# Optimization experiments

Measured on AMD Instinct MI355X. Metric: run time of the kernel, lower is better.

Reference implementation:

```python
import jax, jax.numpy as jnp
import numpy as np

S, B, I, H, O = 512, 64, 256, 1024, 128

def setup_inputs() -> dict:
    key = jax.random.key(0)
    ks = jax.random.split(key, 9)
    std0 = 1.0 / np.sqrt(H)
    inp = {
        "x": jax.random.normal(ks[0], (S, B, I), dtype=jnp.float32),
        "W_r0": jax.random.normal(ks[1], (H, I + H), dtype=jnp.float32) * std0,
        "b_r0": jnp.zeros((H,), jnp.float32),
        "W_z0": jax.random.normal(ks[2], (H, I + H), dtype=jnp.float32) * std0,
        "b_z0": jnp.zeros((H,), jnp.float32),
        "W_h0": jax.random.normal(ks[3], (H, I + H), dtype=jnp.float32) * std0,
        "b_h0": jnp.zeros((H,), jnp.float32),
        "W_r1": jax.random.normal(ks[4], (H, H + H), dtype=jnp.float32) * std0,
        "b_r1": jnp.zeros((H,), jnp.float32),
        "W_z1": jax.random.normal(ks[5], (H, H + H), dtype=jnp.float32) * std0,
        "b_z1": jnp.zeros((H,), jnp.float32),
        "W_h1": jax.random.normal(ks[6], (H, H + H), dtype=jnp.float32) * std0,
        "b_h1": jnp.zeros((H,), jnp.float32),
        "W_out": jax.random.normal(ks[7], (O, H), dtype=jnp.float32) * (1.0 / np.sqrt(H)),
        "b_out": jax.random.normal(ks[8], (O,), dtype=jnp.float32) * (1.0 / np.sqrt(H)),
    }
    return inp

def _gru_cell(x, h, W_r, b_r, W_z, b_z, W_h, b_h):
    # x: [B, in], h: [B, H]
    comb = jnp.concatenate([x, h], axis=1)
    r = jax.nn.sigmoid(comb @ W_r.T + b_r)
    z = jax.nn.sigmoid(comb @ W_z.T + b_z)
    rc = jnp.concatenate([x, r * h], axis=1)
    h_tilde = jnp.tanh(rc @ W_h.T + b_h)
    return (1.0 - z) * h + z * h_tilde

def reference(x, W_r0, b_r0, W_z0, b_z0, W_h0, b_h0,
              W_r1, b_r1, W_z1, b_z1, W_h1, b_h1, W_out, b_out):
    batch = x.shape[1]
    h0_init = jnp.zeros((batch, H), x.dtype)
    h1_init = jnp.zeros((batch, H), x.dtype)

    def step(carry, x_t):
        h0, h1 = carry
        h0 = _gru_cell(x_t, h0, W_r0, b_r0, W_z0, b_z0, W_h0, b_h0)
        h1 = _gru_cell(h0, h1, W_r1, b_r1, W_z1, b_z1, W_h1, b_h1)
        out_t = h1 @ W_out.T + b_out  # [B, O]
        return (h0, h1), out_t

    (h0_f, h1_f), outputs = jax.lax.scan(step, (h0_init, h1_init), x)
    return outputs, jnp.stack([h0_f, h1_f], axis=0)  # [S,B,O], [L,B,H]
```

## Files before the change

### kernel.cpp

```cpp
#include <hip/hip_runtime.h>

#define SLEN 512
#define BATCH 64
#define IDIM 256
#define HDIM 1024
#define ODIM 128
#define NBLK 256
#define NTHR 512
#define AGENT __HIP_MEMORY_SCOPE_AGENT
#define SLOTB 1605632ull

typedef unsigned short ushortT;
typedef unsigned long long ull;
typedef __attribute__((ext_vector_type(8))) short short8;
typedef __attribute__((ext_vector_type(4))) float f32x4;

__device__ __forceinline__ ushortT f2bf(float f) {
  unsigned u = __float_as_uint(f);
  unsigned r = (u + 0x7FFFu + ((u >> 16) & 1u)) >> 16;
  return (ushortT)r;
}

__device__ __forceinline__ void pack2(const float* __restrict__ s, ushortT* d) {
  float4 a = *(const float4*)s;
  float4 b = *(const float4*)(s + 16);
  short8 v;
  v[0]=(short)f2bf(a.x); v[1]=(short)f2bf(a.y); v[2]=(short)f2bf(a.z); v[3]=(short)f2bf(a.w);
  v[4]=(short)f2bf(b.x); v[5]=(short)f2bf(b.y); v[6]=(short)f2bf(b.z); v[7]=(short)f2bf(b.w);
  *(short8*)d = v;
}

__device__ __forceinline__ void pack2a(const float* __restrict__ s, ushortT* d) {
  float4 a = *(const float4*)s;
  float4 b = *(const float4*)(s + 16);
  ull lo = (ull)f2bf(a.x) | ((ull)f2bf(a.y) << 16) | ((ull)f2bf(a.z) << 32) | ((ull)f2bf(a.w) << 48);
  ull hi = (ull)f2bf(b.x) | ((ull)f2bf(b.y) << 16) | ((ull)f2bf(b.z) << 32) | ((ull)f2bf(b.w) << 48);
  __hip_atomic_store((ull*)d, lo, __ATOMIC_RELAXED, AGENT);
  __hip_atomic_store((ull*)(d + 4), hi, __ATOMIC_RELAXED, AGENT);
}

__device__ __forceinline__ void mir_store(ushortT* M, int row, int cL, float v) {
  int kt = cL >> 5, c5 = cL & 31;
  int h = c5 >> 4, g = (c5 >> 2) & 3, j = c5 & 3;
  int u = ((kt * 4 + (row >> 4)) * 64) + 16 * g + (row & 15);
  __hip_atomic_store(&M[(size_t)u * 8 + h * 4 + j], f2bf(v), __ATOMIC_RELAXED, AGENT);
}

__device__ __forceinline__ void st_f32x4(float* p, float v0, float v1, float v2, float v3) {
  ull lo = (ull)__float_as_uint(v0) | ((ull)__float_as_uint(v1) << 32);
  ull hi = (ull)__float_as_uint(v2) | ((ull)__float_as_uint(v3) << 32);
  __hip_atomic_store((ull*)p, lo, __ATOMIC_RELAXED, AGENT);
  __hip_atomic_store((ull*)(p + 2), hi, __ATOMIC_RELAXED, AGENT);
}

__device__ __forceinline__ void gsync(unsigned* sy, int blk, int tid, unsigned idx, bool acq) {
  __syncthreads();
  if (tid == 0)
    __hip_atomic_store(&sy[16 * blk], idx, __ATOMIC_RELAXED, AGENT);
  if (tid < 256) {
    while (__hip_atomic_load(&sy[16 * tid], __ATOMIC_RELAXED, AGENT) < idx)
      __builtin_amdgcn_s_sleep(1);
  }
  __syncthreads();
  if (acq) {
    if (tid == 0) __hip_atomic_load(&sy[16 * blk], __ATOMIC_ACQUIRE, AGENT);
    __syncthreads();
  }
}

__device__ __forceinline__ float fold8(float v) {
  v += __shfl_xor(v, 8);
  v += __shfl_xor(v, 16);
  v += __shfl_xor(v, 32);
  return v;
}

template<int NKT, int SPLIT, int NC>
__device__ __forceinline__ f32x4 stage_mm16(
    const ushortT* __restrict__ mA, const ushortT* __restrict__ mB,
    const ushortT* WL, float (*red)[64][4], int l, int w)
{
  const int mt = w & 3, kh = w >> 2;
  constexpr int H = NKT / 2;
  const int lo = kh * H;
  const int g = l >> 4, col = l & 15;
  f32x4 acc = {0.f, 0.f, 0.f, 0.f};
  short8 af[H];
  #pragma unroll
  for (int t = 0; t < H; ++t) {
    const int kt = lo + t;
    const ushortT* p = (kt < SPLIT)
        ? mA + (size_t)((kt * 4 + mt) * 64 + l) * 8
        : mB + (size_t)(((kt - SPLIT) * 4 + mt) * 64 + l) * 8;
    af[t] = *(const short8*)p;
  }
  #pragma unroll
  for (int t = 0; t < H; ++t) {
    short8 b = {0,0,0,0,0,0,0,0};
    if (col < NC)
      b = *(const short8*)(&WL[(size_t)(((lo + t) * 4 + g) * NC + col) * 8]);
    acc = __builtin_amdgcn_mfma_f32_16x16x32_bf16(af[t], b, acc, 0, 0, 0);
  }
  if (w >= 4) *(f32x4*)&red[w - 4][l][0] = acc;
  __syncthreads();
  if (w < 4) { f32x4 o = *(f32x4*)&red[w][l][0]; acc += o; }
  return acc;
}

__device__ __forceinline__ void out_dot(const ushortT* __restrict__ Mh1p,
                                        const ushortT* WLo, float bo,
                                        float* __restrict__ out,
                                        int s_store, int jo, int tid) {
  const int l = tid & 63, w = tid >> 6;
  const int rr = (w << 3) + (l & 7);
  const int ks = l >> 3;
  const int mt = rr >> 4, r15 = rr & 15;
  float a0 = 0.f;
  #pragma unroll
  for (int q = 0; q < 4; ++q) {
    const int kt = (ks << 2) + q;
    #pragma unroll
    for (int gg = 0; gg < 4; ++gg) {
      const int u = ((kt << 2) + mt) * 64 + (gg << 4) + r15;
      union { short8 v; ushortT us[8]; } M;
      M.v = *(const short8*)(Mh1p + (size_t)u * 8);
      ull wlo = *(const ull*)(WLo + kt * 36 + (gg << 2));
      ull whi = *(const ull*)(WLo + kt * 36 + 16 + (gg << 2));
      #pragma unroll
      for (int j = 0; j < 4; ++j) {
        float mv = __uint_as_float(((unsigned)M.us[j]) << 16);
        float wv = __uint_as_float((unsigned)((wlo >> (16 * j)) & 0xFFFFu) << 16);
        a0 = fmaf(mv, wv, a0);
      }
      #pragma unroll
      for (int j = 0; j < 4; ++j) {
        float mv = __uint_as_float(((unsigned)M.us[4 + j]) << 16);
        float wv = __uint_as_float((unsigned)((whi >> (16 * j)) & 0xFFFFu) << 16);
        a0 = fmaf(mv, wv, a0);
      }
    }
  }
  float v = fold8(a0);
  if ((l & 56) == 0)
    out[((size_t)s_store * BATCH + rr) * ODIM + jo] = v + bo;
}

__global__ __launch_bounds__(NTHR, 2) void gru_pipe(
    const float* __restrict__ x,
    const float* __restrict__ Wr0, const float* __restrict__ br0,
    const float* __restrict__ Wz0, const float* __restrict__ bz0,
    const float* __restrict__ Wh0, const float* __restrict__ bh0,
    const float* __restrict__ Wr1, const float* __restrict__ br1,
    const float* __restrict__ Wz1, const float* __restrict__ bz1,
    const float* __restrict__ Wh1, const float* __restrict__ bh1,
    const float* __restrict__ Wout, const float* __restrict__ bout,
    float* __restrict__ out, char* __restrict__ ws, int nrot)
{
  __shared__ ushortT WSH[53248];
  __shared__ float red[4][64][4];

  const int blk = blockIdx.x;
  const int tid = threadIdx.x;
  const int l = tid & 63;
  const int w = tid >> 6;
  const int g = l >> 4;
  const int colL = l & 15;
  const int rowb = (w << 4) + (g << 2);

  unsigned* sy = (unsigned*)ws;
  char* slots = ws + 16384;

  ushortT* WA = WSH;
  ushortT* WB = WSH + (blk < 128 ? 20480 : 32768);

  if (blk < 128) {
    const int j0 = blk * 8;
    for (int u = tid; u < 40 * 4 * 16; u += NTHR) {
      int kt = u >> 6, gg = (u >> 4) & 3, c = u & 15;
      const float* src = (c < 8 ? Wr0 + (size_t)(j0 + c) * 1280
                                : Wz0 + (size_t)(j0 + c - 8) * 1280) + kt * 32 + gg * 4;
      pack2(src, &WA[(size_t)u * 8]);
    }
  } else {
    const int j1 = (blk - 128) * 8;
    for (int u = tid; u < 64 * 4 * 16; u += NTHR) {
      int kt = u >> 6, gg = (u >> 4) & 3, c = u & 15;
      const float* src = (c < 8 ? Wr1 + (size_t)(j1 + c) * 2048
                                : Wz1 + (size_t)(j1 + c - 8) * 2048) + kt * 32 + gg * 4;
      pack2(src, &WA[(size_t)u * 8]);
    }
  }
  if (blk < 64) {
    const int c0 = blk * 16;
    for (int u = tid; u < 40 * 4 * 16; u += NTHR) {
      int kt = u >> 6, gg = (u >> 4) & 3, c = u & 15;
      pack2(Wh0 + (size_t)(c0 + c) * 1280 + kt * 32 + gg * 4, &WB[(size_t)u * 8]);
    }
  } else if (blk < 128) {
    const int c0 = (blk - 64) * 16;
    for (int u = tid; u < 64 * 4 * 16; u += NTHR) {
      int kt = u >> 6, gg = (u >> 4) & 3, c = u & 15;
      pack2(Wh1 + (size_t)(c0 + c) * 2048 + kt * 32 + gg * 4, &WB[(size_t)u * 8]);
    }
  } else {
    for (int u = tid; u < 256; u += NTHR) {
      float4 a = *(const float4*)(Wout + (size_t)(blk - 128) * HDIM + (u << 2));
      int kt = u >> 3, c4 = (u & 7) << 2;
      ushortT* dst = &WB[kt * 36 + c4];
      dst[0] = f2bf(a.x); dst[1] = f2bf(a.y); dst[2] = f2bf(a.z); dst[3] = f2bf(a.w);
    }
  }
  if (blk >= 128 && tid < 16) {
    ushortT* Mx0 = (ushortT*)(slots + 1572864);
    int u = ((blk - 128) << 4) + tid;
    int kt = u >> 8, mtu = (u >> 6) & 3, lane = u & 63;
    int row = (mtu << 4) + (lane & 15), gg = lane >> 4;
    pack2a(x + (size_t)row * IDIM + (kt << 5) + (gg << 2), Mx0 + (size_t)u * 8);
  }

  float biasA = 0.f, biasB = 0.f, bo = 0.f;
  int cgA = 0, cgB = 0;
  if (blk < 128) {
    cgA = (blk << 3) + (colL & 7);
    biasA = (colL < 8) ? br0[cgA] : bz0[cgA];
  } else {
    cgA = ((blk - 128) << 3) + (colL & 7);
    biasA = (colL < 8) ? br1[cgA] : bz1[cgA];
  }
  if (blk < 64)       { cgB = (blk << 4) + colL;        biasB = bh0[cgB]; }
  else if (blk < 128) { cgB = ((blk - 64) << 4) + colL; biasB = bh1[cgB]; }
  else                { bo = bout[blk - 128]; }

  unsigned sidx = 0;
  gsync(sy, blk, tid, ++sidx, true);

  for (int i = 0; i <= SLEN; ++i) {
    const int pc = i % nrot;
    const int pp = (i + nrot - 1) % nrot;
    const int pn = (i + 1) % nrot;
    char* Spc = slots + SLOTB * pc;
    char* Spp = slots + SLOTB * pp;

    const float* h0prev = (const float*)Spp;
    float*       h0cur  = (float*)Spc;
    const float* h1prev = (const float*)(Spp + 262144);
    float*       h1cur  = (float*)(Spc + 262144);
    float* z0f = (float*)(Spc + 524288);
    float* z1f = (float*)(Spc + 786432);
    const ushortT* Mh0p = (const ushortT*)(Spp + 1048576);
    ushortT*       Mh0w = (ushortT*)(Spc + 1048576);
    const ushortT* Mh1p = (const ushortT*)(Spp + 1179648);
    ushortT*       Mh1w = (ushortT*)(Spc + 1179648);
    ushortT* Mrh0 = (ushortT*)(Spc + 1310720);
    ushortT* Mrh1 = (ushortT*)(Spc + 1441792);
    const ushortT* MxP = (const ushortT*)(Spc + 1572864);
    ushortT*       MxW = (ushortT*)(slots + SLOTB * pn + 1572864);

    if (blk < 128) {
      if (i < SLEN) {
        float4 hq = {0.f, 0.f, 0.f, 0.f};
        if (w < 4 && colL < 8)
          hq = *(const float4*)(h0prev + (size_t)cgA * 64 + rowb);
        f32x4 acc = stage_mm16<40, 8, 16>(MxP, Mh0p, WA, red, l, w);
        if (w < 4) {
          float sg[4];
          #pragma unroll
          for (int r = 0; r < 4; ++r)
            sg[r] = 1.f / (1.f + __expf(-(acc[r] + biasA)));
          if (colL < 8) {
            mir_store(Mrh0, rowb + 0, cgA, sg[0] * hq.x);
            mir_store(Mrh0, rowb + 1, cgA, sg[1] * hq.y);
            mir_store(Mrh0, rowb + 2, cgA, sg[2] * hq.z);
            mir_store(Mrh0, rowb + 3, cgA, sg[3] * hq.w);
          } else {
            st_f32x4(z0f + (size_t)cgA * 64 + rowb, sg[0], sg[1], sg[2], sg[3]);
          }
        }
      }
    } else {
      if (i >= 1) {
        float4 hq = {0.f, 0.f, 0.f, 0.f};
        if (w < 4 && colL < 8)
          hq = *(const float4*)(h1prev + (size_t)cgA * 64 + rowb);
        f32x4 acc = stage_mm16<64, 32, 16>(Mh0p, Mh1p, WA, red, l, w);
        if (w < 4) {
          float sg[4];
          #pragma unroll
          for (int r = 0; r < 4; ++r)
            sg[r] = 1.f / (1.f + __expf(-(acc[r] + biasA)));
          if (colL < 8) {
            mir_store(Mrh1, rowb + 0, cgA, sg[0] * hq.x);
            mir_store(Mrh1, rowb + 1, cgA, sg[1] * hq.y);
            mir_store(Mrh1, rowb + 2, cgA, sg[2] * hq.z);
            mir_store(Mrh1, rowb + 3, cgA, sg[3] * hq.w);
          } else {
            st_f32x4(z1f + (size_t)cgA * 64 + rowb, sg[0], sg[1], sg[2], sg[3]);
          }
        }
      }
    }
    gsync(sy, blk, tid, ++sidx, (i % nrot) == 0);

    if (blk < 64) {
      if (i < SLEN) {
        float4 zq = {0.f, 0.f, 0.f, 0.f}, hq = {0.f, 0.f, 0.f, 0.f};
        if (w < 4) {
          zq = *(const float4*)(z0f + (size_t)cgB * 64 + rowb);
          hq = *(const float4*)(h0prev + (size_t)cgB * 64 + rowb);
        }
        f32x4 acc = stage_mm16<40, 8, 16>(MxP, Mrh0, WB, red, l, w);
        if (w < 4) {
          float hn[4];
          const float hpv[4] = {hq.x, hq.y, hq.z, hq.w};
          const float zv[4] = {zq.x, zq.y, zq.z, zq.w};
          #pragma unroll
          for (int r = 0; r < 4; ++r) {
            float ht = tanhf(acc[r] + biasB);
            hn[r] = fmaf(zv[r], ht - hpv[r], hpv[r]);
            mir_store(Mh0w, rowb + r, cgB, hn[r]);
          }
          st_f32x4(h0cur + (size_t)cgB * 64 + rowb, hn[0], hn[1], hn[2], hn[3]);
        }
      }
    } else if (blk < 128) {
      if (i >= 1) {
        float4 zq = {0.f, 0.f, 0.f, 0.f}, hq = {0.f, 0.f, 0.f, 0.f};
        if (w < 4) {
          zq = *(const float4*)(z1f + (size_t)cgB * 64 + rowb);
          hq = *(const float4*)(h1prev + (size_t)cgB * 64 + rowb);
        }
        f32x4 acc = stage_mm16<64, 32, 16>(Mh0p, Mrh1, WB, red, l, w);
        if (w < 4) {
          float hn[4];
          const float hpv[4] = {hq.x, hq.y, hq.z, hq.w};
          const float zv[4] = {zq.x, zq.y, zq.z, zq.w};
          #pragma unroll
          for (int r = 0; r < 4; ++r) {
            float ht = tanhf(acc[r] + biasB);
            hn[r] = fmaf(zv[r], ht - hpv[r], hpv[r]);
            mir_store(Mh1w, rowb + r, cgB, hn[r]);
          }
          st_f32x4(h1cur + (size_t)cgB * 64 + rowb, hn[0], hn[1], hn[2], hn[3]);
        }
      }
    } else {
      if (i + 1 < SLEN && tid < 16) {
        int u = ((blk - 128) << 4) + tid;
        int kt = u >> 8, mtu = (u >> 6) & 3, lane = u & 63;
        int row = (mtu << 4) + (lane & 15), gg = lane >> 4;
        pack2a(x + ((size_t)(i + 1) * BATCH + row) * IDIM + (kt << 5) + (gg << 2),
               MxW + (size_t)u * 8);
      }
      if (i >= 2)
        out_dot(Mh1p, WB, bo, out, i - 2, blk - 128, tid);
    }
    gsync(sy, blk, tid, ++sidx, ((i + 1) % nrot) == 0 || i == SLEN);
  }

  {
    char* Sf1 = slots + SLOTB * (SLEN % nrot);
    char* Sf0 = slots + SLOTB * ((SLEN - 1) % nrot);
    if (blk >= 128)
      out_dot((const ushortT*)(Sf1 + 1179648), WB, bo, out, SLEN - 1, blk - 128, tid);
    const float* h0fin = (const float*)Sf0;
    const float* h1fin = (const float*)(Sf1 + 262144);
    const size_t base = (size_t)SLEN * BATCH * ODIM;
    const int u = blk * NTHR + tid;
    float v;
    if (u < 65536) {
      int row = u >> 10, col = u & 1023;
      v = h0fin[(size_t)col * 64 + row];
    } else {
      int t = u - 65536;
      int row = t >> 10, col = t & 1023;
      v = h1fin[(size_t)col * 64 + row];
    }
    out[base + u] = v;
  }
}

extern "C" void kernel_launch(void* const* d_in, const int* in_sizes, int n_in,
                              void* d_out, int out_size, void* d_ws, size_t ws_size,
                              hipStream_t stream) {
  const float* xx  = (const float*)d_in[0];
  const float* Wr0 = (const float*)d_in[1];
  const float* br0 = (const float*)d_in[2];
  const float* Wz0 = (const float*)d_in[3];
  const float* bz0 = (const float*)d_in[4];
  const float* Wh0 = (const float*)d_in[5];
  const float* bh0 = (const float*)d_in[6];
  const float* Wr1 = (const float*)d_in[7];
  const float* br1 = (const float*)d_in[8];
  const float* Wz1 = (const float*)d_in[9];
  const float* bz1 = (const float*)d_in[10];
  const float* Wh1 = (const float*)d_in[11];
  const float* bh1 = (const float*)d_in[12];
  const float* Wou = (const float*)d_in[13];
  const float* bou = (const float*)d_in[14];

  long long avail = (long long)ws_size - 16384;
  int nrot = (int)(avail / (long long)SLOTB);
  if (nrot > 8) nrot = 8;
  if (nrot < 2) nrot = 2;

  hipMemsetAsync(d_ws, 0, 16384 + (size_t)nrot * SLOTB, stream);

  gru_pipe<<<dim3(NBLK), dim3(NTHR), 0, stream>>>(
      xx, Wr0, br0, Wz0, bz0, Wh0, bh0,
      Wr1, br1, Wz1, bz1, Wh1, bh1, Wou, bou,
      (float*)d_out, (char*)d_ws, nrot);
}
```

Baseline: 7.174 ms.

## Split persistent GRU into layer groups with partial barriers instead of global grid sync

Reassigns the 256 blocks into four 64-block roles: layer-0 gates, layer-0 candidate, layer-1 gates plus output projection, and layer-1 candidate. Each block holds a single weight slice rather than two, and the r and z gates are computed together per block with two MFMA accumulators. The full-grid barrier is replaced by per-layer barriers over 128 blocks plus targeted cross-group waits, so layer 0 and layer 1 run loosely coupled rather than in lockstep. This removes a whole-grid spin wait from each step, at the cost of more delicate ordering between slots, which could break if nrot is small.

```diff
diff --git a/kernel.cpp b/kernel.cpp
--- a/kernel.cpp
+++ b/kernel.cpp
@@ -53,29 +53,27 @@
   __hip_atomic_store((ull*)(p + 2), hi, __ATOMIC_RELAXED, AGENT);
 }
 
-__device__ __forceinline__ void gsync(unsigned* sy, int blk, int tid, unsigned idx, bool acq) {
+__device__ __forceinline__ void ewait(unsigned* sy, int base, int n, unsigned tgt, int tid) {
+  if (tid < n)
+    while (__hip_atomic_load(&sy[16 * (base + tid)], __ATOMIC_RELAXED, AGENT) < tgt)
+      __builtin_amdgcn_s_sleep(1);
+  __syncthreads();
+}
+
+__device__ __forceinline__ void psync(unsigned* sy, int blk, int tid, unsigned idx,
+                                      int wbase, int wn) {
   __syncthreads();
   if (tid == 0)
     __hip_atomic_store(&sy[16 * blk], idx, __ATOMIC_RELAXED, AGENT);
-  if (tid < 256) {
-    while (__hip_atomic_load(&sy[16 * tid], __ATOMIC_RELAXED, AGENT) < idx)
+  if (tid < wn)
+    while (__hip_atomic_load(&sy[16 * (wbase + tid)], __ATOMIC_RELAXED, AGENT) < idx)
       __builtin_amdgcn_s_sleep(1);
-  }
-  __syncthreads();
-  if (acq) {
-    if (tid == 0) __hip_atomic_load(&sy[16 * blk], __ATOMIC_ACQUIRE, AGENT);
-    __syncthreads();
-  }
-}
-
-__device__ __forceinline__ float fold8(float v) {
-  v += __shfl_xor(v, 8);
-  v += __shfl_xor(v, 16);
-  v += __shfl_xor(v, 32);
-  return v;
-}
-
-template<int NKT, int SPLIT, int NC>
+  __syncthreads();
+  if (tid == 0) __hip_atomic_load(&sy[16 * blk], __ATOMIC_ACQUIRE, AGENT);
+  __syncthreads();
+}
+
+template<int NKT, int SPLIT>
 __device__ __forceinline__ f32x4 stage_mm16(
     const ushortT* __restrict__ mA, const ushortT* __restrict__ mB,
     const ushortT* WL, float (*red)[64][4], int l, int w)
@@ -96,9 +94,7 @@
   }
   #pragma unroll
   for (int t = 0; t < H; ++t) {
-    short8 b = {0,0,0,0,0,0,0,0};
-    if (col < NC)
-      b = *(const short8*)(&WL[(size_t)(((lo + t) * 4 + g) * NC + col) * 8]);
+    short8 b = *(const short8*)(&WL[(size_t)(((lo + t) * 4 + g) * 16 + col) * 8]);
     acc = __builtin_amdgcn_mfma_f32_16x16x32_bf16(af[t], b, acc, 0, 0, 0);
   }
   if (w >= 4) *(f32x4*)&red[w - 4][l][0] = acc;
@@ -107,18 +103,59 @@
   return acc;
 }
 
-__device__ __forceinline__ void out_dot(const ushortT* __restrict__ Mh1p,
-                                        const ushortT* WLo, float bo,
-                                        float* __restrict__ out,
-                                        int s_store, int jo, int tid) {
-  const int l = tid & 63, w = tid >> 6;
-  const int rr = (w << 3) + (l & 7);
-  const int ks = l >> 3;
-  const int mt = rr >> 4, r15 = rr & 15;
+template<int NKT, int SPLIT>
+__device__ __forceinline__ void stage_gates(
+    const ushortT* __restrict__ mA, const ushortT* __restrict__ mB,
+    const ushortT* WL, float (*redR)[64][4], float (*redZ)[64][4],
+    int l, int w, f32x4& accR, f32x4& accZ)
+{
+  const int mt = w & 3, kh = w >> 2;
+  constexpr int H = NKT / 2;
+  const int lo = kh * H;
+  const int g = l >> 4, col = l & 15;
+  accR = (f32x4){0.f, 0.f, 0.f, 0.f};
+  accZ = (f32x4){0.f, 0.f, 0.f, 0.f};
+  short8 af[H];
+  #pragma unroll
+  for (int t = 0; t < H; ++t) {
+    const int kt = lo + t;
+    const ushortT* p = (kt < SPLIT)
+        ? mA + (size_t)((kt * 4 + mt) * 64 + l) * 8
+        : mB + (size_t)(((kt - SPLIT) * 4 + mt) * 64 + l) * 8;
+    af[t] = *(const short8*)p;
+  }
+  #pragma unroll
+  for (int t = 0; t < H; ++t) {
+    const int kt = lo + t;
+    short8 bR = *(const short8*)(&WL[(size_t)((kt * 4 + g) * 32 + col) * 8]);
+    short8 bZ = *(const short8*)(&WL[(size_t)((kt * 4 + g) * 32 + 16 + col) * 8]);
+    accR = __builtin_amdgcn_mfma_f32_16x16x32_bf16(af[t], bR, accR, 0, 0, 0);
+    accZ = __builtin_amdgcn_mfma_f32_16x16x32_bf16(af[t], bZ, accZ, 0, 0, 0);
+  }
+  if (w >= 4) {
+    *(f32x4*)&redR[w - 4][l][0] = accR;
+    *(f32x4*)&redZ[w - 4][l][0] = accZ;
+  }
+  __syncthreads();
+  if (w < 4) {
+    accR += *(f32x4*)&redR[w][l][0];
+    accZ += *(f32x4*)&redZ[w][l][0];
+  }
+}
+
+__device__ __forceinline__ void out_dot2(const ushortT* __restrict__ Mh1p,
+                                         const ushortT* WLO, const float* __restrict__ bout,
+                                         float* __restrict__ out,
+                                         int s_store, int jo_base, int l, int w) {
+  const int cc = w >> 2;
+  const int mt = w & 3;
+  const int r15 = l & 15;
+  const int ks = l >> 4;
+  const ushortT* WLo = WLO + cc * 1152;
   float a0 = 0.f;
   #pragma unroll
-  for (int q = 0; q < 4; ++q) {
-    const int kt = (ks << 2) + q;
+  for (int q = 0; q < 8; ++q) {
+    const int kt = (ks << 3) + q;
     #pragma unroll
     for (int gg = 0; gg < 4; ++gg) {
       const int u = ((kt << 2) + mt) * 64 + (gg << 4) + r15;
@@ -127,25 +164,25 @@
       ull wlo = *(const ull*)(WLo + kt * 36 + (gg << 2));
       ull whi = *(const ull*)(WLo + kt * 36 + 16 + (gg << 2));
       #pragma unroll
-      for (int j = 0; j < 4; ++j) {
-        float mv = __uint_as_float(((unsigned)M.us[j]) << 16);
-        float wv = __uint_as_float((unsigned)((wlo >> (16 * j)) & 0xFFFFu) << 16);
-        a0 = fmaf(mv, wv, a0);
-      }
+      for (int j = 0; j < 4; ++j)
+        a0 = fmaf(__uint_as_float(((unsigned)M.us[j]) << 16),
+                  __uint_as_float((unsigned)((wlo >> (16 * j)) & 0xFFFFu) << 16), a0);
       #pragma unroll
-      for (int j = 0; j < 4; ++j) {
-        float mv = __uint_as_float(((unsigned)M.us[4 + j]) << 16);
-        float wv = __uint_as_float((unsigned)((whi >> (16 * j)) & 0xFFFFu) << 16);
-        a0 = fmaf(mv, wv, a0);
-      }
-    }
-  }
-  float v = fold8(a0);
-  if ((l & 56) == 0)
-    out[((size_t)s_store * BATCH + rr) * ODIM + jo] = v + bo;
-}
-
-__global__ __launch_bounds__(NTHR, 2) void gru_pipe(
+      for (int j = 0; j < 4; ++j)
+        a0 = fmaf(__uint_as_float(((unsigned)M.us[4 + j]) << 16),
+                  __uint_as_float((unsigned)((whi >> (16 * j)) & 0xFFFFu) << 16), a0);
+    }
+  }
+  a0 += __shfl_xor(a0, 16);
+  a0 += __shfl_xor(a0, 32);
+  if (ks == 0) {
+    const int rr = (mt << 4) + r15;
+    const int jo = jo_base + cc;
+    out[((size_t)s_store * BATCH + rr) * ODIM + jo] = a0 + bout[jo];
+  }
+}
+
+__global__ __launch_bounds__(NTHR, 2) void gru_flow(
     const float* __restrict__ x,
     const float* __restrict__ Wr0, const float* __restrict__ br0,
     const float* __restrict__ Wz0, const float* __restrict__ bz0,
@@ -156,225 +193,215 @@
     const float* __restrict__ Wout, const float* __restrict__ bout,
     float* __restrict__ out, char* __restrict__ ws, int nrot)
 {
-  __shared__ ushortT WSH[53248];
-  __shared__ float red[4][64][4];
+  __shared__ ushortT WSH[65536];
+  __shared__ ushortT WLO[2304];
+  __shared__ float redA[4][64][4];
+  __shared__ float redB[4][64][4];
 
   const int blk = blockIdx.x;
   const int tid = threadIdx.x;
   const int l = tid & 63;
   const int w = tid >> 6;
-  const int g = l >> 4;
   const int colL = l & 15;
-  const int rowb = (w << 4) + (g << 2);
+  const int rowb = ((w & 3) << 4) + ((l >> 4) << 2);
+
+  const bool isG0 = (blk < 64);
+  const bool isC0 = (blk >= 64 && blk < 128);
+  const bool isG1 = (blk >= 128 && blk < 192);
+  const int dbase = (blk < 128) ? 0 : 128;
 
   unsigned* sy = (unsigned*)ws;
   char* slots = ws + 16384;
 
-  ushortT* WA = WSH;
-  ushortT* WB = WSH + (blk < 128 ? 20480 : 32768);
-
-  if (blk < 128) {
-    const int j0 = blk * 8;
+  if (isG0) {
+    const int cb = blk * 16;
+    for (int u = tid; u < 40 * 4 * 32; u += NTHR) {
+      int kt = u >> 7, gg = (u >> 5) & 3, c = u & 31;
+      const float* src = (c < 16 ? Wr0 + (size_t)(cb + c) * 1280
+                                 : Wz0 + (size_t)(cb + c - 16) * 1280) + kt * 32 + gg * 4;
+      pack2(src, &WSH[(size_t)u * 8]);
+    }
+    if (tid < 32) {
+      ushortT* Mx0 = (ushortT*)(slots + 1572864);
+      int u = blk * 32 + tid;
+      int kt = u >> 8, mtu = (u >> 6) & 3, lane = u & 63;
+      int row = (mtu << 4) + (lane & 15), gg = lane >> 4;
+      pack2a(x + (size_t)row * IDIM + (kt << 5) + (gg << 2), Mx0 + (size_t)u * 8);
+    }
+  } else if (isC0) {
+    const int cb = (blk - 64) * 16;
     for (int u = tid; u < 40 * 4 * 16; u += NTHR) {
       int kt = u >> 6, gg = (u >> 4) & 3, c = u & 15;
-      const float* src = (c < 8 ? Wr0 + (size_t)(j0 + c) * 1280
-                                : Wz0 + (size_t)(j0 + c - 8) * 1280) + kt * 32 + gg * 4;
-      pack2(src, &WA[(size_t)u * 8]);
+      pack2(Wh0 + (size_t)(cb + c) * 1280 + kt * 32 + gg * 4, &WSH[(size_t)u * 8]);
+    }
+  } else if (isG1) {
+    const int cb = (blk - 128) * 16;
+    for (int u = tid; u < 64 * 4 * 32; u += NTHR) {
+      int kt = u >> 7, gg = (u >> 5) & 3, c = u & 31;
+      const float* src = (c < 16 ? Wr1 + (size_t)(cb + c) * 2048
+                                 : Wz1 + (size_t)(cb + c - 16) * 2048) + kt * 32 + gg * 4;
+      pack2(src, &WSH[(size_t)u * 8]);
+    }
+    for (int u = tid; u < 512; u += NTHR) {
+      int cc = u >> 8, v = u & 255;
+      float4 a = *(const float4*)(Wout + (size_t)((blk - 128) * 2 + cc) * HDIM + (v << 2));
+      int kt = v >> 3, c4 = (v & 7) << 2;
+      ushortT* dst = &WLO[cc * 1152 + kt * 36 + c4];
+      dst[0] = f2bf(a.x); dst[1] = f2bf(a.y); dst[2] = f2bf(a.z); dst[3] = f2bf(a.w);
     }
   } else {
-    const int j1 = (blk - 128) * 8;
+    const int cb = (blk - 192) * 16;
     for (int u = tid; u < 64 * 4 * 16; u += NTHR) {
       int kt = u >> 6, gg = (u >> 4) & 3, c = u & 15;
-      const float* src = (c < 8 ? Wr1 + (size_t)(j1 + c) * 2048
-                                : Wz1 + (size_t)(j1 + c - 8) * 2048) + kt * 32 + gg * 4;
-      pack2(src, &WA[(size_t)u * 8]);
-    }
-  }
-  if (blk < 64) {
-    const int c0 = blk * 16;
-    for (int u = tid; u < 40 * 4 * 16; u += NTHR) {
-      int kt = u >> 6, gg = (u >> 4) & 3, c = u & 15;
-      pack2(Wh0 + (size_t)(c0 + c) * 1280 + kt * 32 + gg * 4, &WB[(size_t)u * 8]);
-    }
-  } else if (blk < 128) {
-    const int c0 = (blk - 64) * 16;
-    for (int u = tid; u < 64 * 4 * 16; u += NTHR) {
-      int kt = u >> 6, gg = (u >> 4) & 3, c = u & 15;
-      pack2(Wh1 + (size_t)(c0 + c) * 2048 + kt * 32 + gg * 4, &WB[(size_t)u * 8]);
-    }
+      pack2(Wh1 + (size_t)(cb + c) * 2048 + kt * 32 + gg * 4, &WSH[(size_t)u * 8]);
+    }
+  }
+
+  float biasR = 0.f, biasZ = 0.f, biasB = 0.f;
+  int cgA = 0, cgB = 0, job = 0;
+  if (isG0) {
+    cgA = blk * 16 + colL; biasR = br0[cgA]; biasZ = bz0[cgA];
+  } else if (isC0) {
+    cgB = (blk - 64) * 16 + colL; biasB = bh0[cgB];
+  } else if (isG1) {
+    cgA = (blk - 128) * 16 + colL; biasR = br1[cgA]; biasZ = bz1[cgA];
+    job = (blk - 128) * 2;
   } else {
-    for (int u = tid; u < 256; u += NTHR) {
-      float4 a = *(const float4*)(Wout + (size_t)(blk - 128) * HDIM + (u << 2));
-      int kt = u >> 3, c4 = (u & 7) << 2;
-      ushortT* dst = &WB[kt * 36 + c4];
-      dst[0] = f2bf(a.x); dst[1] = f2bf(a.y); dst[2] = f2bf(a.z); dst[3] = f2bf(a.w);
-    }
-  }
-  if (blk >= 128 && tid < 16) {
-    ushortT* Mx0 = (ushortT*)(slots + 1572864);
-    int u = ((blk - 128) << 4) + tid;
-    int kt = u >> 8, mtu = (u >> 6) & 3, lane = u & 63;
-    int row = (mtu << 4) + (lane & 15), gg = lane >> 4;
-    pack2a(x + (size_t)row * IDIM + (kt << 5) + (gg << 2), Mx0 + (size_t)u * 8);
-  }
-
-  float biasA = 0.f, biasB = 0.f, bo = 0.f;
-  int cgA = 0, cgB = 0;
-  if (blk < 128) {
-    cgA = (blk << 3) + (colL & 7);
-    biasA = (colL < 8) ? br0[cgA] : bz0[cgA];
-  } else {
-    cgA = ((blk - 128) << 3) + (colL & 7);
-    biasA = (colL < 8) ? br1[cgA] : bz1[cgA];
-  }
-  if (blk < 64)       { cgB = (blk << 4) + colL;        biasB = bh0[cgB]; }
-  else if (blk < 128) { cgB = ((blk - 64) << 4) + colL; biasB = bh1[cgB]; }
-  else                { bo = bout[blk - 128]; }
-
-  unsigned sidx = 0;
-  gsync(sy, blk, tid, ++sidx, true);
-
-  for (int i = 0; i <= SLEN; ++i) {
-    const int pc = i % nrot;
-    const int pp = (i + nrot - 1) % nrot;
-    const int pn = (i + 1) % nrot;
-    char* Spc = slots + SLOTB * pc;
-    char* Spp = slots + SLOTB * pp;
-
-    const float* h0prev = (const float*)Spp;
-    float*       h0cur  = (float*)Spc;
-    const float* h1prev = (const float*)(Spp + 262144);
-    float*       h1cur  = (float*)(Spc + 262144);
-    float* z0f = (float*)(Spc + 524288);
-    float* z1f = (float*)(Spc + 786432);
-    const ushortT* Mh0p = (const ushortT*)(Spp + 1048576);
-    ushortT*       Mh0w = (ushortT*)(Spc + 1048576);
-    const ushortT* Mh1p = (const ushortT*)(Spp + 1179648);
-    ushortT*       Mh1w = (ushortT*)(Spc + 1179648);
-    ushortT* Mrh0 = (ushortT*)(Spc + 1310720);
-    ushortT* Mrh1 = (ushortT*)(Spc + 1441792);
-    const ushortT* MxP = (const ushortT*)(Spc + 1572864);
-    ushortT*       MxW = (ushortT*)(slots + SLOTB * pn + 1572864);
-
-    if (blk < 128) {
-      if (i < SLEN) {
-        float4 hq = {0.f, 0.f, 0.f, 0.f};
-        if (w < 4 && colL < 8)
-          hq = *(const float4*)(h0prev + (size_t)cgA * 64 + rowb);
-        f32x4 acc = stage_mm16<40, 8, 16>(MxP, Mh0p, WA, red, l, w);
-        if (w < 4) {
-          float sg[4];
-          #pragma unroll
-          for (int r = 0; r < 4; ++r)
-            sg[r] = 1.f / (1.f + __expf(-(acc[r] + biasA)));
-          if (colL < 8) {
-            mir_store(Mrh0, rowb + 0, cgA, sg[0] * hq.x);
-            mir_store(Mrh0, rowb + 1, cgA, sg[1] * hq.y);
-            mir_store(Mrh0, rowb + 2, cgA, sg[2] * hq.z);
-            mir_store(Mrh0, rowb + 3, cgA, sg[3] * hq.w);
-          } else {
-            st_f32x4(z0f + (size_t)cgA * 64 + rowb, sg[0], sg[1], sg[2], sg[3]);
-          }
+    cgB = (blk - 192) * 16 + colL; biasB = bh1[cgB];
+  }
+
+  psync(sy, blk, tid, 1u, 0, 256);
+
+  for (int k = 0; k < SLEN; ++k) {
+    const int sc = k % nrot;
+    const int sp = (k + nrot - 1) % nrot;
+    char* Sc = slots + SLOTB * sc;
+    char* Sp = slots + SLOTB * sp;
+    float*       h0c = (float*)Sc;
+    const float* h0p = (const float*)Sp;
+    float*       h1c = (float*)(Sc + 262144);
+    const float* h1p = (const float*)(Sp + 262144);
+    float* z0c = (float*)(Sc + 524288);
+    float* z1c = (float*)(Sc + 786432);
+    ushortT*       Mh0c  = (ushortT*)(Sc + 1048576);
+    const ushortT* Mh0pv = (const ushortT*)(Sp + 1048576);
+    ushortT*       Mh1c  = (ushortT*)(Sc + 1179648);
+    const ushortT* Mh1pv = (const ushortT*)(Sp + 1179648);
+    ushortT* Mrh0 = (ushortT*)(Sc + 1310720);
+    ushortT* Mrh1 = (ushortT*)(Sc + 1441792);
+    const ushortT* MxC = (const ushortT*)(Sc + 1572864);
+    ushortT* MxN = (ushortT*)(slots + SLOTB * ((k + 1) % nrot) + 1572864);
+
+    if (isG0) {
+      float4 hq = {0.f, 0.f, 0.f, 0.f};
+      if (w < 4) hq = *(const float4*)(h0p + (size_t)cgA * 64 + rowb);
+      f32x4 aR, aZ;
+      stage_gates<40, 8>(MxC, Mh0pv, WSH, redA, redB, l, w, aR, aZ);
+      if (w < 4) {
+        float sgR[4], sgZ[4];
+        #pragma unroll
+        for (int r = 0; r < 4; ++r) {
+          sgR[r] = 1.f / (1.f + __expf(-(aR[r] + biasR)));
+          sgZ[r] = 1.f / (1.f + __expf(-(aZ[r] + biasZ)));
         }
-      }
-    } else {
-      if (i >= 1) {
-        float4 hq = {0.f, 0.f, 0.f, 0.f};
-        if (w < 4 && colL < 8)
-          hq = *(const float4*)(h1prev + (size_t)cgA * 64 + rowb);
-        f32x4 acc = stage_mm16<64, 32, 16>(Mh0p, Mh1p, WA, red, l, w);
-        if (w < 4) {
-          float sg[4];
-          #pragma unroll
-          for (int r = 0; r < 4; ++r)
-            sg[r] = 1.f / (1.f + __expf(-(acc[r] + biasA)));
-          if (colL < 8) {
-            mir_store(Mrh1, rowb + 0, cgA, sg[0] * hq.x);
-            mir_store(Mrh1, rowb + 1, cgA, sg[1] * hq.y);
-            mir_store(Mrh1, rowb + 2, cgA, sg[2] * hq.z);
-            mir_store(Mrh1, rowb + 3, cgA, sg[3] * hq.w);
-          } else {
-            st_f32x4(z1f + (size_t)cgA * 64 + rowb, sg[0], sg[1], sg[2], sg[3]);
-          }
+        mir_store(Mrh0, rowb + 0, cgA, sgR[0] * hq.x);
+        mir_store(Mrh0, rowb + 1, cgA, sgR[1] * hq.y);
+        mir_store(Mrh0, rowb + 2, cgA, sgR[2] * hq.z);
+        mir_store(Mrh0, rowb + 3, cgA, sgR[3] * hq.w);
+        st_f32x4(z0c + (size_t)cgA * 64 + rowb, sgZ[0], sgZ[1], sgZ[2], sgZ[3]);
+      }
+    } else if (isC0) {
+      if (k >= nrot) ewait(sy, 192, 64, 2u * (unsigned)(k - nrot) + 3u, tid);
+    } else if (isG1) {
+      ewait(sy, 64, 64, 2u * (unsigned)k + 3u, tid);
+      float4 hq = {0.f, 0.f, 0.f, 0.f};
+      if (w < 4) hq = *(const float4*)(h1p + (size_t)cgA * 64 + rowb);
+      f32x4 aR, aZ;
+      stage_gates<64, 32>(Mh0c, Mh1pv, WSH, redA, redB, l, w, aR, aZ);
+      if (w < 4) {
+        float sgR[4], sgZ[4];
+        #pragma unroll
+        for (int r = 0; r < 4; ++r) {
+          sgR[r] = 1.f / (1.f + __expf(-(aR[r] + biasR)));
+          sgZ[r] = 1.f / (1.f + __expf(-(aZ[r] + biasZ)));
         }
-      }
-    }
-    gsync(sy, blk, tid, ++sidx, (i % nrot) == 0);
-
-    if (blk < 64) {
-      if (i < SLEN) {
-        float4 zq = {0.f, 0.f, 0.f, 0.f}, hq = {0.f, 0.f, 0.f, 0.f};
-        if (w < 4) {
-          zq = *(const float4*)(z0f + (size_t)cgB * 64 + rowb);
-          hq = *(const float4*)(h0prev + (size_t)cgB * 64 + rowb);
-        }
-        f32x4 acc = stage_mm16<40, 8, 16>(MxP, Mrh0, WB, red, l, w);
-        if (w < 4) {
-          float hn[4];
-          const float hpv[4] = {hq.x, hq.y, hq.z, hq.w};
-          const float zv[4] = {zq.x, zq.y, zq.z, zq.w};
-          #pragma unroll
-          for (int r = 0; r < 4; ++r) {
-            float ht = tanhf(acc[r] + biasB);
-            hn[r] = fmaf(zv[r], ht - hpv[r], hpv[r]);
-            mir_store(Mh0w, rowb + r, cgB, hn[r]);
-          }
-          st_f32x4(h0cur + (size_t)cgB * 64 + rowb, hn[0], hn[1], hn[2], hn[3]);
-        }
-      }
-    } else if (blk < 128) {
-      if (i >= 1) {
-        float4 zq = {0.f, 0.f, 0.f, 0.f}, hq = {0.f, 0.f, 0.f, 0.f};
-        if (w < 4) {
-          zq = *(const float4*)(z1f + (size_t)cgB * 64 + rowb);
-          hq = *(const float4*)(h1prev + (size_t)cgB * 64 + rowb);
-        }
-        f32x4 acc = stage_mm16<64, 32, 16>(Mh0p, Mrh1, WB, red, l, w);
-        if (w < 4) {
-          float hn[4];
-          const float hpv[4] = {hq.x, hq.y, hq.z, hq.w};
-          const float zv[4] = {zq.x, zq.y, zq.z, zq.w};
-          #pragma unroll
-          for (int r = 0; r < 4; ++r) {
-            float ht = tanhf(acc[r] + biasB);
-            hn[r] = fmaf(zv[r], ht - hpv[r], hpv[r]);
-            mir_store(Mh1w, rowb + r, cgB, hn[r]);
-          }
-          st_f32x4(h1cur + (size_t)cgB * 64 + rowb, hn[0], hn[1], hn[2], hn[3]);
-        }
-      }
-    } else {
-      if (i + 1 < SLEN && tid < 16) {
-        int u = ((blk - 128) << 4) + tid;
+        mir_store(Mrh1, rowb + 0, cgA, sgR[0] * hq.x);
+        mir_store(Mrh1, rowb + 1, cgA, sgR[1] * hq.y);
+        mir_store(Mrh1, rowb + 2, cgA, sgR[2] * hq.z);
+        mir_store(Mrh1, rowb + 3, cgA, sgR[3] * hq.w);
+        st_f32x4(z1c + (size_t)cgA * 64 + rowb, sgZ[0], sgZ[1], sgZ[2], sgZ[3]);
+      }
+    }
+    psync(sy, blk, tid, 2u * (unsigned)k + 2u, dbase, 128);
+
+    if (isG0) {
+      if (k + 1 < SLEN && tid < 32) {
+        int u = blk * 32 + tid;
         int kt = u >> 8, mtu = (u >> 6) & 3, lane = u & 63;
         int row = (mtu << 4) + (lane & 15), gg = lane >> 4;
-        pack2a(x + ((size_t)(i + 1) * BATCH + row) * IDIM + (kt << 5) + (gg << 2),
-               MxW + (size_t)u * 8);
-      }
-      if (i >= 2)
-        out_dot(Mh1p, WB, bo, out, i - 2, blk - 128, tid);
-    }
-    gsync(sy, blk, tid, ++sidx, ((i + 1) % nrot) == 0 || i == SLEN);
-  }
+        pack2a(x + ((size_t)(k + 1) * BATCH + row) * IDIM + (kt << 5) + (gg << 2),
+               MxN + (size_t)u * 8);
+      }
+    } else if (isC0) {
+      float4 zq = {0.f, 0.f, 0.f, 0.f}, hq = {0.f, 0.f, 0.f, 0.f};
+      if (w < 4) {
+        zq = *(const float4*)(z0c + (size_t)cgB * 64 + rowb);
+        hq = *(const float4*)(h0p + (size_t)cgB * 64 + rowb);
+      }
+      f32x4 acc = stage_mm16<40, 8>(MxC, Mrh0, WSH, redA, l, w);
+      if (w < 4) {
+        const float hpv[4] = {hq.x, hq.y, hq.z, hq.w};
+        const float zv[4] = {zq.x, zq.y, zq.z, zq.w};
+        float hn[4];
+        #pragma unroll
+        for (int r = 0; r < 4; ++r) {
+          float ht = tanhf(acc[r] + biasB);
+          hn[r] = fmaf(zv[r], ht - hpv[r], hpv[r]);
+          mir_store(Mh0c, rowb + r, cgB, hn[r]);
+        }
+        st_f32x4(h0c + (size_t)cgB * 64 + rowb, hn[0], hn[1], hn[2], hn[3]);
+      }
+    } else if (isG1) {
+      if (k >= 1) out_dot2(Mh1pv, WLO, bout, out, k - 1, job, l, w);
+    } else {
+      float4 zq = {0.f, 0.f, 0.f, 0.f}, hq = {0.f, 0.f, 0.f, 0.f};
+      if (w < 4) {
+        zq = *(const float4*)(z1c + (size_t)cgB * 64 + rowb);
+        hq = *(const float4*)(h1p + (size_t)cgB * 64 + rowb);
+      }
+      f32x4 acc = stage_mm16<64, 32>(Mh0c, Mrh1, WSH, redA, l, w);
+      if (w < 4) {
+        const float hpv[4] = {hq.x, hq.y, hq.z, hq.w};
+        const float zv[4] = {zq.x, zq.y, zq.z, zq.w};
+        float hn[4];
+        #pragma unroll
+        for (int r = 0; r < 4; ++r) {
+          float ht = tanhf(acc[r] + biasB);
+          hn[r] = fmaf(zv[r], ht - hpv[r], hpv[r]);
+          mir_store(Mh1c, rowb + r, cgB, hn[r]);
+        }
+        st_f32x4(h1c + (size_t)cgB * 64 + rowb, hn[0], hn[1], hn[2], hn[3]);
+      }
+    }
+    psync(sy, blk, tid, 2u * (unsigned)k + 3u, dbase, 128);
+  }
+
+  ewait(sy, 0, 256, 2u * (unsigned)(SLEN - 1) + 3u, tid);
+  if (tid == 0) __hip_atomic_load(&sy[16 * blk], __ATOMIC_ACQUIRE, AGENT);
+  __syncthreads();
 
   {
-    char* Sf1 = slots + SLOTB * (SLEN % nrot);
-    char* Sf0 = slots + SLOTB * ((SLEN - 1) % nrot);
-    if (blk >= 128)
-      out_dot((const ushortT*)(Sf1 + 1179648), WB, bo, out, SLEN - 1, blk - 128, tid);
-    const float* h0fin = (const float*)Sf0;
-    const float* h1fin = (const float*)(Sf1 + 262144);
+    const int sf = (SLEN - 1) % nrot;
+    char* Sf = slots + SLOTB * sf;
+    if (isG1)
+      out_dot2((const ushortT*)(Sf + 1179648), WLO, bout, out, SLEN - 1, job, l, w);
+    const float* h0fin = (const float*)Sf;
+    const float* h1fin = (const float*)(Sf + 262144);
     const size_t base = (size_t)SLEN * BATCH * ODIM;
     const int u = blk * NTHR + tid;
     float v;
-    if (u < 65536) {
-      int row = u >> 10, col = u & 1023;
-      v = h0fin[(size_t)col * 64 + row];
-    } else {
-      int t = u - 65536;
-      int row = t >> 10, col = t & 1023;
-      v = h1fin[(size_t)col * 64 + row];
-    }
+    if (u < 65536) { int row = u >> 10, col = u & 1023; v = h0fin[(size_t)col * 64 + row]; }
+    else { int t = u - 65536; int row = t >> 10, col = t & 1023; v = h1fin[(size_t)col * 64 + row]; }
     out[base + u] = v;
   }
 }
@@ -405,7 +432,7 @@
 
   hipMemsetAsync(d_ws, 0, 16384 + (size_t)nrot * SLOTB, stream);
 
-  gru_pipe<<<dim3(NBLK), dim3(NTHR), 0, stream>>>(
+  gru_flow<<<dim3(NBLK), dim3(NTHR), 0, stream>>>(
       xx, Wr0, br0, Wz0, bz0, Wh0, bh0,
       Wr1, br1, Wz1, bz1, Wh1, bh1, Wou, bou,
       (float*)d_out, (char*)d_ws, nrot);
```

Result: slower. 11.16 ms (+55.6%).
